# Optimization experiments

Measured on AMD Instinct MI355X. Metric: run time of the kernel, lower is better.

## Reference

```python
import jax, jax.numpy as jnp
import numpy as np

EPS = 1e-3  # batch_norm_epsilon


def _lstm_last(xs, W, U, b):
    """Keras-order LSTM (gates i,f,g,o); returns last hidden state [B,H]."""
    B = xs.shape[0]
    H = U.shape[0]

    def step(carry, xt):
        h, c = carry
        z = xt @ W + h @ U + b  # [B, 4H]
        i, f, g, o = jnp.split(z, 4, axis=-1)
        i = jax.nn.sigmoid(i)
        f = jax.nn.sigmoid(f)
        g = jnp.tanh(g)
        o = jax.nn.sigmoid(o)
        c = f * c + i * g
        h = o * jnp.tanh(c)
        return (h, c), None

    init = (jnp.zeros((B, H), xs.dtype), jnp.zeros((B, H), xs.dtype))
    (h, _), _ = jax.lax.scan(step, init, jnp.swapaxes(xs, 0, 1))
    return h


def setup_inputs() -> dict:
    key = jax.random.key(0)
    ks = jax.random.split(key, 10)
    B, T, C, H = 32, 512, 512, 512
    s_in = 1.0 / np.sqrt(C)
    s_rec = 1.0 / np.sqrt(H)
    return {
        "x": jax.random.normal(ks[0], (B, T, C), jnp.float32),
        # BatchNorm params (inference / moving stats)
        "gamma": jnp.ones((C,), jnp.float32),
        "beta": jnp.zeros((C,), jnp.float32),
        "moving_mean": jax.random.normal(ks[1], (C,), jnp.float32) * 0.1,
        "moving_var": jnp.abs(jax.random.normal(ks[2], (C,), jnp.float32)) * 0.1 + 1.0,
        # forward-direction LSTM
        "Wf": jax.random.normal(ks[3], (C, 4 * H), jnp.float32) * s_in,
        "Uf": jax.random.normal(ks[4], (H, 4 * H), jnp.float32) * s_rec,
        "bf": jnp.zeros((4 * H,), jnp.float32),
        # backward-direction LSTM
        "Wb": jax.random.normal(ks[5], (C, 4 * H), jnp.float32) * s_in,
        "Ub": jax.random.normal(ks[6], (H, 4 * H), jnp.float32) * s_rec,
        "bb": jnp.zeros((4 * H,), jnp.float32),
    }


def reference(x, gamma, beta, moving_mean, moving_var, Wf, Uf, bf, Wb, Ub, bb):
    # BatchNorm (inference) over last axis
    inv = jax.lax.rsqrt(moving_var + EPS)
    xn = (x - moving_mean) * inv * gamma + beta
    # Bidirectional LSTM, merge_mode='concat', return_sequences=False
    h_fwd = _lstm_last(xn, Wf, Uf, bf)
    h_bwd = _lstm_last(xn[:, ::-1, :], Wb, Ub, bb)
    return jnp.concatenate([h_fwd, h_bwd], axis=-1)  # [B, 2H]
```

## Files before the change

### kernel.cpp

```cpp
#include <hip/hip_runtime.h>
#include <stdint.h>

typedef __attribute__((ext_vector_type(8))) short short8;
typedef __attribute__((ext_vector_type(4))) float f32x4;
typedef __attribute__((ext_vector_type(2))) float f32x2;
typedef __attribute__((ext_vector_type(4))) unsigned int u32x4;
typedef __attribute__((ext_vector_type(2))) unsigned int u32x2;

#define NB 32
#define NBH 16
#define NT 512
#define NC 512
#define NH 512
#define NG 2048
#define WPG 16
#define NWG 64
#define UPW 32

__device__ __forceinline__ float bf2f(unsigned short u){
  union { unsigned int i; float f; } v; v.i = ((unsigned int)u) << 16; return v.f;
}
__device__ __forceinline__ unsigned short f2bf(float f){
  union { float f; unsigned int i; } v; v.f = f;
  unsigned int r = v.i + 0x7fffu + ((v.i >> 16) & 1u);
  return (unsigned short)(r >> 16);
}
__device__ __forceinline__ bool dt_fp32(const void* gamma){
  return ((const unsigned short*)gamma)[0] != 0x3F80;
}
__device__ __forceinline__ float ldv(const void* p, size_t i, bool f32){
  return f32 ? ((const float*)p)[i] : bf2f(((const unsigned short*)p)[i]);
}
__device__ __forceinline__ short8 frag_from_f32(const float* p){
  short8 r;
  #pragma unroll
  for (int j = 0; j < 8; ++j) r[j] = (short)f2bf(p[j]);
  return r;
}
__device__ __forceinline__ float sigm(float x){ return 1.f/(1.f + __expf(-x)); }
__device__ __forceinline__ float tanh_(float x){ return 1.f - 2.f/(1.f + __expf(2.f*x)); }

__device__ __forceinline__ unsigned int permhi(unsigned int hi, unsigned int lo){
  return __builtin_amdgcn_perm(hi, lo, 0x07060302u);
}

__device__ __forceinline__ void tag_load(const unsigned int* p0, u32x4 r[8]){
  asm volatile(
    "global_load_dwordx4 %0, %8, off sc0 sc1\n\t"
    "global_load_dwordx4 %1, %8, off offset:16 sc0 sc1\n\t"
    "global_load_dwordx4 %2, %8, off offset:128 sc0 sc1\n\t"
    "global_load_dwordx4 %3, %8, off offset:144 sc0 sc1\n\t"
    "global_load_dwordx4 %4, %8, off offset:256 sc0 sc1\n\t"
    "global_load_dwordx4 %5, %8, off offset:272 sc0 sc1\n\t"
    "global_load_dwordx4 %6, %8, off offset:384 sc0 sc1\n\t"
    "global_load_dwordx4 %7, %8, off offset:400 sc0 sc1\n\t"
    "s_waitcnt vmcnt(0)"
    : "=&v"(r[0]), "=&v"(r[1]), "=&v"(r[2]), "=&v"(r[3]),
      "=&v"(r[4]), "=&v"(r[5]), "=&v"(r[6]), "=&v"(r[7])
    : "v"(p0) : "memory");
}
__device__ __forceinline__ void tag_store(unsigned int* p, unsigned int lo, unsigned int hi){
  u32x2 v; v[0] = lo; v[1] = hi;
  asm volatile("global_store_dwordx2 %0, %1, off sc0 sc1" :: "v"(p), "v"(v) : "memory");
}

__global__ void k_init(const void* __restrict__ gamma,
                       const void* __restrict__ beta,
                       const void* __restrict__ mmean,
                       const void* __restrict__ mvar,
                       float* __restrict__ scale, float* __restrict__ shift,
                       unsigned int* __restrict__ hbuf){
  bool f32 = dt_fp32(gamma);
  int tid = blockIdx.x * 256 + threadIdx.x;
  if (blockIdx.x == 0){
    for (int c = threadIdx.x; c < NC; c += 256){
      float s = ldv(gamma, c, f32) * rsqrtf(ldv(mvar, c, f32) + 1e-3f);
      scale[c] = s;
      shift[c] = ldv(beta, c, f32) - ldv(mmean, c, f32) * s;
    }
  }
  for (int i = tid; i < 4*2*NBH*NH; i += gridDim.x * 256) hbuf[i] = 0u;
}

__global__ void k_xcast(const void* __restrict__ x, const void* __restrict__ gamma,
                        unsigned short* __restrict__ x2){
  bool f32 = dt_fp32(gamma);
  int i = blockIdx.x * 256 + threadIdx.x;
  int c8 = i & 63;
  int rest = i >> 6;
  int t = rest & (NT - 1);
  int b = rest >> 9;
  size_t src = ((size_t)b * NT + t) * NC + c8 * 8;
  size_t dst = ((size_t)t * NB + b) * NC + c8 * 8;
  unsigned int pk[4];
  if (f32){
    const float* p = (const float*)x + src;
    #pragma unroll
    for (int j = 0; j < 4; ++j)
      pk[j] = (unsigned int)f2bf(p[2*j]) | ((unsigned int)f2bf(p[2*j+1]) << 16);
  } else {
    __builtin_memcpy(pk, (const unsigned short*)x + src, 16);
  }
  __builtin_memcpy(x2 + dst, pk, 16);
}

__global__ __launch_bounds__(256, 1) void k_lstm(
    const void* __restrict__ x, const unsigned short* __restrict__ x2, int use_x2,
    const void* __restrict__ Wf, const void* __restrict__ Uf,
    const void* __restrict__ Wb, const void* __restrict__ Ub,
    const void* __restrict__ bfv, const void* __restrict__ bbv,
    const void* __restrict__ gamma,
    const float* __restrict__ scale, const float* __restrict__ shift,
    unsigned int* __restrict__ hbuf, void* __restrict__ out){
  __shared__ float zbuf[4][NBH][132];
  __shared__ float fscr[256];
  __shared__ float fb[128];

  bool f32 = dt_fp32(gamma);
  int wg   = blockIdx.x;
  int dir  = wg & 1;
  int half = (wg >> 1) & 1;
  int wgd  = wg >> 2;
  int gidx = wg & 3;
  int ubase = wgd * UPW;
  const void* W = dir ? Wb : Wf;
  const void* U = dir ? Ub : Uf;
  const void* bvec = dir ? bbv : bfv;
  int tid  = threadIdx.x;
  int lane = tid & 63, wave = tid >> 6;
  int m = lane & 15, q = lane >> 4;

  short8 bw[4][8], bu[4][8];
  #pragma unroll
  for (int kcl = 0; kcl < 4; ++kcl){
    int kc = wave * 4 + kcl;
    #pragma unroll
    for (int nt = 0; nt < 8; ++nt){
      int col = (nt >> 1) * NH + ubase + (nt & 1) * 16 + m;
      short8 vw, vu;
      #pragma unroll
      for (int j = 0; j < 8; ++j){
        int k = kc * 32 + q * 8 + j;
        vu[j] = (short)f2bf(ldv(U, (size_t)k * NG + col, f32));
        vw[j] = (short)f2bf(scale[k] * ldv(W, (size_t)k * NG + col, f32));
      }
      bw[kcl][nt] = vw; bu[kcl][nt] = vu;
    }
  }

  {
    int cidx = tid >> 1, kh = tid & 1;
    int col = (cidx >> 5) * NH + ubase + (cidx & 31);
    float a = 0.f;
    for (int k = kh * 256; k < kh * 256 + 256; ++k)
      a += shift[k] * ldv(W, (size_t)k * NG + col, f32);
    fscr[tid] = a;
    __syncthreads();
    if (tid < 128)
      fb[tid] = fscr[2*tid] + fscr[2*tid+1]
              + ldv(bvec, (tid >> 5) * NH + ubase + (tid & 31), f32);
    __syncthreads();
  }

  int pb = tid >> 4, pu2 = (tid & 15) * 2;
  float bias_r[2][4];
  #pragma unroll
  for (int j = 0; j < 2; ++j)
    #pragma unroll
    for (int g = 0; g < 4; ++g) bias_r[j][g] = fb[g * 32 + pu2 + j];
  float cst[2] = {0.f, 0.f};

  unsigned int* hb32 = hbuf + (size_t)gidx * 2 * NBH * NH;

  short8 xf[4];
  {
    int tt0 = dir ? (NT - 1) : 0;
    int b = half * 16 + m;
    #pragma unroll
    for (int kcl = 0; kcl < 4; ++kcl){
      int kc = wave * 4 + kcl;
      if (use_x2){
        size_t xi = ((size_t)tt0 * NB + b) * NC + kc * 32 + q * 8;
        __builtin_memcpy(&xf[kcl], x2 + xi, 16);
      } else {
        size_t xi = ((size_t)b * NT + tt0) * NC + kc * 32 + q * 8;
        if (f32) xf[kcl] = frag_from_f32((const float*)x + xi);
        else     __builtin_memcpy(&xf[kcl], (const unsigned short*)x + xi, 16);
      }
    }
  }

  int dly = 100;

  #pragma unroll 1
  for (int t = 0; t < NT; ++t){
    const unsigned int* hcur = hb32 + (size_t)(t & 1) * NBH * NH;
    unsigned int* hnext = hb32 + (size_t)((t + 1) & 1) * NBH * NH;

    f32x4 acc[8];
    #pragma unroll
    for (int nt = 0; nt < 8; ++nt) acc[nt] = (f32x4){0.f,0.f,0.f,0.f};

    #pragma unroll
    for (int kcl = 0; kcl < 4; ++kcl)
      #pragma unroll
      for (int nt = 0; nt < 8; ++nt)
        acc[nt] = __builtin_amdgcn_mfma_f32_16x16x32_bf16(xf[kcl], bw[kcl][nt], acc[nt], 0, 0, 0);

    if (t < NT - 1){
      int ttn = dir ? (NT - 2 - t) : (t + 1);
      int b = half * 16 + m;
      #pragma unroll
      for (int kcl = 0; kcl < 4; ++kcl){
        int kc = wave * 4 + kcl;
        if (use_x2){
          size_t xi = ((size_t)ttn * NB + b) * NC + kc * 32 + q * 8;
          __builtin_memcpy(&xf[kcl], x2 + xi, 16);
        } else {
          size_t xi = ((size_t)b * NT + ttn) * NC + kc * 32 + q * 8;
          if (f32) xf[kcl] = frag_from_f32((const float*)x + xi);
          else     __builtin_memcpy(&xf[kcl], (const unsigned short*)x + xi, 16);
        }
      }
    }
    __builtin_amdgcn_sched_barrier(0);

    u32x4 raw[8];
    {
      unsigned int tg = (unsigned int)t;
      if (t > 0 && dly > 0){
        unsigned long long t0 = __builtin_amdgcn_s_memrealtime();
        while ((unsigned long long)(__builtin_amdgcn_s_memrealtime() - t0)
               < (unsigned long long)dly) {}
      }
      const unsigned int* p0 = hcur + (size_t)m * NH + wave * 128 + q * 8;
      int tries = 0;
      while (true){
        tag_load(p0, raw);
        unsigned int d = 0;
        #pragma unroll
        for (int i = 0; i < 8; ++i)
          d |= (raw[i][0] ^ tg) | (raw[i][1] ^ tg) | (raw[i][2] ^ tg) | (raw[i][3] ^ tg);
        if (__all((int)((d & 0xffffu) == 0u))) break;
        ++tries;
      }
      if (t > 0){
        dly += tries ? 20 : -1;
        if (dly < 0) dly = 0;
        if (dly > 300) dly = 300;
      }
    }

    #pragma unroll
    for (int kcl = 0; kcl < 4; ++kcl){
      union { short8 s; unsigned int w[4]; } u;
      u32x4 a = raw[2 * kcl];
      u32x4 b = raw[2 * kcl + 1];
      u.w[0] = permhi(a[1], a[0]);
      u.w[1] = permhi(a[3], a[2]);
      u.w[2] = permhi(b[1], b[0]);
      u.w[3] = permhi(b[3], b[2]);
      #pragma unroll
      for (int nt = 0; nt < 8; ++nt)
        acc[nt] = __builtin_amdgcn_mfma_f32_16x16x32_bf16(u.s, bu[kcl][nt], acc[nt], 0, 0, 0);
    }

    #pragma unroll
    for (int nt = 0; nt < 8; ++nt){
      int cb = (nt >> 1) * 32 + (nt & 1) * 16 + m;
      #pragma unroll
      for (int r = 0; r < 4; ++r)
        zbuf[wave][q * 4 + r][cb] = acc[nt][r];
    }
    __syncthreads();

    float z[2][4];
    #pragma unroll
    for (int g = 0; g < 4; ++g){ z[0][g] = bias_r[0][g]; z[1][g] = bias_r[1][g]; }
    #pragma unroll
    for (int w = 0; w < 4; ++w)
      #pragma unroll
      for (int g = 0; g < 4; ++g){
        f32x2 v = *(const f32x2*)&zbuf[w][pb][g * 32 + pu2];
        z[0][g] += v[0]; z[1][g] += v[1];
      }
    float hv[2];
    #pragma unroll
    for (int j = 0; j < 2; ++j){
      float iv = sigm(z[j][0]), fv = sigm(z[j][1]), gv = tanh_(z[j][2]), ov = sigm(z[j][3]);
      cst[j] = fv * cst[j] + iv * gv;
      hv[j] = ov * tanh_(cst[j]);
    }

    if (t == NT - 1){
      size_t o0 = (size_t)(half * 16 + pb) * (2 * NH) + dir * NH + ubase + pu2;
      if (f32){
        f32x2 ov2 = {hv[0], hv[1]};
        *(f32x2*)&((float*)out)[o0] = ov2;
      } else {
        unsigned int pk = (unsigned int)f2bf(hv[0]) | ((unsigned int)f2bf(hv[1]) << 16);
        *(unsigned int*)&((unsigned short*)out)[o0] = pk;
      }
      break;
    }

    {
      unsigned int tag1 = (unsigned int)(t + 1);
      unsigned int w0 = ((unsigned int)f2bf(hv[0]) << 16) | tag1;
      unsigned int w1 = ((unsigned int)f2bf(hv[1]) << 16) | tag1;
      tag_store(hnext + (size_t)pb * NH + ubase + pu2, w0, w1);
    }
  }
}

extern "C" void kernel_launch(void* const* d_in, const int* in_sizes, int n_in,
                              void* d_out, int out_size, void* d_ws, size_t ws_size,
                              hipStream_t stream){
  const void* x     = d_in[0];
  const void* gamma = d_in[1];
  const void* beta  = d_in[2];
  const void* mmean = d_in[3];
  const void* mvar  = d_in[4];
  const void* Wf    = d_in[5];
  const void* Uf    = d_in[6];
  const void* bfv   = d_in[7];
  const void* Wb    = d_in[8];
  const void* Ub    = d_in[9];
  const void* bbv   = d_in[10];

  char* ws = (char*)d_ws;
  float* scale = (float*)(ws + 0);
  float* shift = (float*)(ws + 2048);
  unsigned int* hbuf = (unsigned int*)(ws + 20480);
  size_t x2_off = 20480 + 262144 + 4096;
  unsigned short* x2 = (unsigned short*)(ws + x2_off);
  size_t x2_bytes = (size_t)NT * NB * NC * 2;
  int use_x2 = (ws_size >= x2_off + x2_bytes) ? 1 : 0;

  hipLaunchKernelGGL(k_init, dim3(64),  dim3(256), 0, stream,
                     gamma, beta, mmean, mvar, scale, shift, hbuf);
  if (use_x2)
    hipLaunchKernelGGL(k_xcast, dim3((NB*NT*NC/8)/256), dim3(256), 0, stream,
                       x, gamma, x2);
  hipLaunchKernelGGL(k_lstm, dim3(NWG), dim3(256), 0, stream,
                     x, x2, use_x2, Wf, Uf, Wb, Ub, bfv, bbv, gamma, scale, shift,
                     hbuf, d_out);
}
```

Before: 2.002 ms.

## Replace adaptive-delay tag polling with per-workgroup step flags before hidden-state load

Each workgroup now publishes its completed step number to a small flag array after storing its hidden-state slice. Consumers first spin on the 16 flags of their group with one dword load per lane, then do the tagged hidden-state load, which is kept as a correctness check. The adaptive real-time delay loop is removed, and the next-step x prefetch is moved after the wait. This is meant to cut polling traffic and wasted delay on the recurrent critical path. In exchange it adds a serial flag-load round trip before the data load each step.

```diff
diff --git a/kernel.cpp b/kernel.cpp
--- a/kernel.cpp
+++ b/kernel.cpp
@@ -44,6 +44,15 @@
   return __builtin_amdgcn_perm(hi, lo, 0x07060302u);
 }
 
+__device__ __forceinline__ unsigned int llc_load_u32(const unsigned int* p){
+  unsigned int r;
+  asm volatile("global_load_dword %0, %1, off sc0 sc1\n\ts_waitcnt vmcnt(0)"
+               : "=v"(r) : "v"(p) : "memory");
+  return r;
+}
+__device__ __forceinline__ void llc_store_u32(unsigned int* p, unsigned int v){
+  asm volatile("global_store_dword %0, %1, off sc0 sc1" :: "v"(p), "v"(v) : "memory");
+}
 __device__ __forceinline__ void tag_load(const unsigned int* p0, u32x4 r[8]){
   asm volatile(
     "global_load_dwordx4 %0, %8, off sc0 sc1\n\t"
@@ -69,7 +78,7 @@
                        const void* __restrict__ mmean,
                        const void* __restrict__ mvar,
                        float* __restrict__ scale, float* __restrict__ shift,
-                       unsigned int* __restrict__ hbuf){
+                       unsigned int* __restrict__ hbuf, unsigned int* __restrict__ flags){
   bool f32 = dt_fp32(gamma);
   int tid = blockIdx.x * 256 + threadIdx.x;
   if (blockIdx.x == 0){
@@ -78,6 +87,7 @@
       scale[c] = s;
       shift[c] = ldv(beta, c, f32) - ldv(mmean, c, f32) * s;
     }
+    if (threadIdx.x < 128) flags[threadIdx.x] = 0u;
   }
   for (int i = tid; i < 4*2*NBH*NH; i += gridDim.x * 256) hbuf[i] = 0u;
 }
@@ -111,7 +121,8 @@
     const void* __restrict__ bfv, const void* __restrict__ bbv,
     const void* __restrict__ gamma,
     const float* __restrict__ scale, const float* __restrict__ shift,
-    unsigned int* __restrict__ hbuf, void* __restrict__ out){
+    unsigned int* __restrict__ hbuf, unsigned int* __restrict__ flags,
+    void* __restrict__ out){
   __shared__ float zbuf[4][NBH][132];
   __shared__ float fscr[256];
   __shared__ float fb[128];
@@ -170,6 +181,8 @@
     for (int g = 0; g < 4; ++g) bias_r[j][g] = fb[g * 32 + pu2 + j];
   float cst[2] = {0.f, 0.f};
 
+  unsigned int* gflags  = flags + gidx * 32;
+  unsigned int* ownflag = gflags + wgd;
   unsigned int* hb32 = hbuf + (size_t)gidx * 2 * NBH * NH;
 
   short8 xf[4];
@@ -190,8 +203,6 @@
     }
   }
 
-  int dly = 100;
-
   #pragma unroll 1
   for (int t = 0; t < NT; ++t){
     const unsigned int* hcur = hb32 + (size_t)(t & 1) * NBH * NH;
@@ -206,6 +217,28 @@
       #pragma unroll
       for (int nt = 0; nt < 8; ++nt)
         acc[nt] = __builtin_amdgcn_mfma_f32_16x16x32_bf16(xf[kcl], bw[kcl][nt], acc[nt], 0, 0, 0);
+
+    if (t > 0){
+      unsigned int tgt = (unsigned int)t;
+      while (true){
+        unsigned int v = llc_load_u32(gflags + (lane & 15));
+        if (__all((int)(v >= tgt))) break;
+      }
+    }
+
+    u32x4 raw[8];
+    {
+      unsigned int tg = (unsigned int)t;
+      const unsigned int* p0 = hcur + (size_t)m * NH + wave * 128 + q * 8;
+      while (true){
+        tag_load(p0, raw);
+        unsigned int d = 0;
+        #pragma unroll
+        for (int i = 0; i < 8; ++i)
+          d |= (raw[i][0] ^ tg) | (raw[i][1] ^ tg) | (raw[i][2] ^ tg) | (raw[i][3] ^ tg);
+        if (__all((int)((d & 0xffffu) == 0u))) break;
+      }
+    }
 
     if (t < NT - 1){
       int ttn = dir ? (NT - 2 - t) : (t + 1);
@@ -223,33 +256,6 @@
         }
       }
     }
-    __builtin_amdgcn_sched_barrier(0);
-
-    u32x4 raw[8];
-    {
-      unsigned int tg = (unsigned int)t;
-      if (t > 0 && dly > 0){
-        unsigned long long t0 = __builtin_amdgcn_s_memrealtime();
-        while ((unsigned long long)(__builtin_amdgcn_s_memrealtime() - t0)
-               < (unsigned long long)dly) {}
-      }
-      const unsigned int* p0 = hcur + (size_t)m * NH + wave * 128 + q * 8;
-      int tries = 0;
-      while (true){
-        tag_load(p0, raw);
-        unsigned int d = 0;
-        #pragma unroll
-        for (int i = 0; i < 8; ++i)
-          d |= (raw[i][0] ^ tg) | (raw[i][1] ^ tg) | (raw[i][2] ^ tg) | (raw[i][3] ^ tg);
-        if (__all((int)((d & 0xffffu) == 0u))) break;
-        ++tries;
-      }
-      if (t > 0){
-        dly += tries ? 20 : -1;
-        if (dly < 0) dly = 0;
-        if (dly > 300) dly = 300;
-      }
-    }
 
     #pragma unroll
     for (int kcl = 0; kcl < 4; ++kcl){
@@ -309,6 +315,7 @@
       unsigned int w0 = ((unsigned int)f2bf(hv[0]) << 16) | tag1;
       unsigned int w1 = ((unsigned int)f2bf(hv[1]) << 16) | tag1;
       tag_store(hnext + (size_t)pb * NH + ubase + pu2, w0, w1);
+      if (tid == 0) llc_store_u32(ownflag, tag1);
     }
   }
 }
@@ -331,18 +338,19 @@
   char* ws = (char*)d_ws;
   float* scale = (float*)(ws + 0);
   float* shift = (float*)(ws + 2048);
-  unsigned int* hbuf = (unsigned int*)(ws + 20480);
+  unsigned int* hbuf  = (unsigned int*)(ws + 20480);
+  unsigned int* flags = (unsigned int*)(ws + 20480 + 262144);
   size_t x2_off = 20480 + 262144 + 4096;
   unsigned short* x2 = (unsigned short*)(ws + x2_off);
   size_t x2_bytes = (size_t)NT * NB * NC * 2;
   int use_x2 = (ws_size >= x2_off + x2_bytes) ? 1 : 0;
 
   hipLaunchKernelGGL(k_init, dim3(64),  dim3(256), 0, stream,
-                     gamma, beta, mmean, mvar, scale, shift, hbuf);
+                     gamma, beta, mmean, mvar, scale, shift, hbuf, flags);
   if (use_x2)
     hipLaunchKernelGGL(k_xcast, dim3((NB*NT*NC/8)/256), dim3(256), 0, stream,
                        x, gamma, x2);
   hipLaunchKernelGGL(k_lstm, dim3(NWG), dim3(256), 0, stream,
                      x, x2, use_x2, Wf, Uf, Wb, Ub, bfv, bbv, gamma, scale, shift,
-                     hbuf, d_out);
-}
+                     hbuf, flags, d_out);
+}
```

New measurement: 1.974 ms. About the same (-1.4%).
